# Performance work log

Hardware: AMD Instinct MI355X
Metric: run time of the kernel (lower is better)

## Reference

```python
import math
import jax, jax.numpy as jnp
import numpy as np

B, N, C, H = 64, 197, 768, 12
KEEP_RATE = 0.7

def setup_inputs() -> dict:
    key = jax.random.key(0)
    k0, k1, k2 = jax.random.split(key, 3)
    x = jax.random.normal(k0, (B, N, C), jnp.float32)
    qkv_w = jax.random.normal(k1, (C, 3 * C), jnp.float32) * 0.02
    qkv_b = jnp.zeros((3 * C,), jnp.float32)
    proj_w = jax.random.normal(k2, (C, C), jnp.float32) * 0.02
    proj_b = jnp.zeros((C,), jnp.float32)
    return {"x": x, "qkv_w": qkv_w, "qkv_b": qkv_b, "proj_w": proj_w, "proj_b": proj_b}

def reference(x, qkv_w, qkv_b, proj_w, proj_b):
    b, n, c = x.shape
    d = c // H
    scale = d ** -0.5
    # qkv: [B,N,3C] -> [3,B,H,N,d]
    qkv = (x @ qkv_w + qkv_b).reshape(b, n, 3, H, d)
    qkv = jnp.transpose(qkv, (2, 0, 3, 1, 4))
    q, k, v = qkv[0], qkv[1], qkv[2]
    attn = jax.nn.softmax(jnp.einsum('bhnd,bhmd->bhnm', q, k) * scale, axis=-1)  # [B,H,N,N]
    out = jnp.einsum('bhnm,bhmd->bhnd', attn, v)          # [B,H,N,d]
    out = jnp.transpose(out, (0, 2, 1, 3)).reshape(b, n, c)
    x_out = out @ proj_w + proj_b                          # [B,N,C]
    # dynamic token pruning via CLS attention (row 0, excluding CLS itself)
    left_tokens = math.ceil(KEEP_RATE * (n - 1))
    cls_attn = attn[:, :, 0, 1:].mean(axis=1)              # [B,N-1]
    _, idx = jax.lax.top_k(cls_attn, left_tokens)          # descending, sorted
    index = jnp.broadcast_to(idx[:, :, None], (b, left_tokens, c))
    return (x_out, index, idx, cls_attn, left_tokens)
```

## Files before the change

kernel.cpp:

```cpp
#include <hip/hip_runtime.h>
#include <math.h>

#define BB   64
#define NTOK 197
#define CC   768
#define HH   12
#define DH   64
#define MTOT (BB * NTOK)
#define MPAD 12672
#define LEFT 138

#define XOUT_OFF  0
#define INDEX_OFF 9682944
#define IDX_OFF   16465920
#define CLS_OFF   16474752
#define LT_OFF    16487296

typedef short s8v __attribute__((ext_vector_type(8)));
typedef short s4v __attribute__((ext_vector_type(4)));
typedef float f4v __attribute__((ext_vector_type(4)));

#define GLOAD16(g, l) __builtin_amdgcn_global_load_lds( \
    (const __attribute__((address_space(1))) unsigned int*)(g), \
    (__attribute__((address_space(3))) unsigned int*)(l), 16, 0, 0)

__device__ __forceinline__ unsigned short f2bf(float f) {
    union { float f; unsigned int i; } x; x.f = f;
    unsigned int r = x.i + 0x7FFFu + ((x.i >> 16) & 1u);
    return (unsigned short)(r >> 16);
}

__global__ __launch_bounds__(256)
void convert_x(const float* __restrict__ in, unsigned short* __restrict__ outb)
{
    size_t i = ((size_t)blockIdx.x * 256 + threadIdx.x) * 8;
    float4 a = *(const float4*)(in + i);
    float4 b = *(const float4*)(in + i + 4);
    s8v r;
    r[0] = (short)f2bf(a.x); r[1] = (short)f2bf(a.y);
    r[2] = (short)f2bf(a.z); r[3] = (short)f2bf(a.w);
    r[4] = (short)f2bf(b.x); r[5] = (short)f2bf(b.y);
    r[6] = (short)f2bf(b.z); r[7] = (short)f2bf(b.w);
    *(s8v*)(outb + i) = r;
}

__global__ __launch_bounds__(256)
void transpose_w2(const float* __restrict__ inq, const float* __restrict__ inp,
                  unsigned short* __restrict__ outq, unsigned short* __restrict__ outp)
{
    __shared__ float tile[32][33];
    const int bi = blockIdx.x;
    int bj = blockIdx.y;
    const float* in; unsigned short* outb; int N;
    if (bj < 72) { in = inq; outb = outq; N = 2304; }
    else         { bj -= 72; in = inp; outb = outp; N = 768; }
    const int tx = threadIdx.x & 31, ty = threadIdx.x >> 5;
#pragma unroll
    for (int r = ty; r < 32; r += 8)
        tile[r][tx] = in[(size_t)(bi * 32 + r) * N + bj * 32 + tx];
    __syncthreads();
#pragma unroll
    for (int r = ty; r < 32; r += 8)
        outb[(size_t)(bj * 32 + r) * 768 + bi * 32 + tx] = f2bf(tile[tx][r]);
}

__global__ __launch_bounds__(256, 3)
void gemm_bf16(const unsigned short* __restrict__ A, const unsigned short* __restrict__ BT,
               const float* __restrict__ bias, int ncolt, int mode, int rt0, int nrt,
               unsigned short* __restrict__ outb, float* __restrict__ outf)
{
    const int id = blockIdx.x;
    const int xcd = id & 7;
    const int t = id >> 3;
    const int ct = t % ncolt, s = t / ncolt;
    const int rt = s * 8 + xcd;
    if (rt >= nrt) return;
    const int m0 = (rt0 + rt) * 128, n0 = ct * 128;

    const int tid = threadIdx.x;
    const int wave = tid >> 6, lane = tid & 63;
    const int quad = lane >> 4, l16 = lane & 15;
    const int rowbase = (wave >> 1) * 64, colbase = (wave & 1) * 64;
    __shared__ __align__(16) short As[128 * 64];
    __shared__ __align__(16) short Bs[128 * 64];

    const int rA   = lane >> 3;
    const int gcol = ((lane & 7) ^ rA) * 8;
    unsigned int agof[4], bgof[4];
#pragma unroll
    for (int i = 0; i < 4; ++i) {
        int c = wave * 4 + i;
        agof[i] = (unsigned int)((m0 + c * 8 + rA) * 768 + gcol);
        bgof[i] = (unsigned int)((n0 + c * 8 + rA) * 768 + gcol);
    }
    int aoff[4], boff[4];
#pragma unroll
    for (int i = 0; i < 4; ++i) {
        aoff[i] = (rowbase + i * 16 + l16) * 64 + ((quad ^ (l16 & 7)) * 8);
        boff[i] = (colbase + i * 16 + l16) * 64 + ((quad ^ (l16 & 7)) * 8);
    }

    f4v acc[4][4];
#pragma unroll
    for (int i = 0; i < 4; ++i)
#pragma unroll
        for (int j = 0; j < 4; ++j) acc[i][j] = (f4v)0.f;

    for (int k0 = 0; k0 < 768; k0 += 64) {
#pragma unroll
        for (int i = 0; i < 4; ++i) {
            int c = wave * 4 + i;
            GLOAD16(A  + agof[i] + k0, &As[c * 512]);
            GLOAD16(BT + bgof[i] + k0, &Bs[c * 512]);
        }
        __syncthreads();
#pragma unroll
        for (int ks = 0; ks < 2; ++ks) {
            const int x = ks * 32;
            s8v af[4], bf[4];
#pragma unroll
            for (int i = 0; i < 4; ++i) af[i] = *(const s8v*)&As[aoff[i] ^ x];
#pragma unroll
            for (int j = 0; j < 4; ++j) bf[j] = *(const s8v*)&Bs[boff[j] ^ x];
#pragma unroll
            for (int i = 0; i < 4; ++i)
#pragma unroll
                for (int j = 0; j < 4; ++j)
                    acc[i][j] = __builtin_amdgcn_mfma_f32_16x16x32_bf16(bf[j], af[i], acc[i][j], 0, 0, 0);
        }
        __syncthreads();
    }

    const int ncols = mode ? 768 : 2304;
#pragma unroll
    for (int i = 0; i < 4; ++i) {
        const int m = m0 + rowbase + i * 16 + l16;
        if (m >= MTOT) continue;
#pragma unroll
        for (int j = 0; j < 4; ++j) {
            const int nb = n0 + colbase + j * 16 + quad * 4;
            float4 b4 = *(const float4*)&bias[nb];
            if (mode == 1) {
                float4 r;
                r.x = acc[i][j][0] + b4.x; r.y = acc[i][j][1] + b4.y;
                r.z = acc[i][j][2] + b4.z; r.w = acc[i][j][3] + b4.w;
                *(float4*)(outf + (size_t)m * ncols + nb) = r;
            } else {
                s4v r;
                r[0] = (short)f2bf(acc[i][j][0] + b4.x);
                r[1] = (short)f2bf(acc[i][j][1] + b4.y);
                r[2] = (short)f2bf(acc[i][j][2] + b4.z);
                r[3] = (short)f2bf(acc[i][j][3] + b4.w);
                *(s4v*)(outb + (size_t)m * ncols + nb) = r;
            }
        }
    }
}

#define VTS 224

__global__ __launch_bounds__(256)
void transpose_v(const unsigned short* __restrict__ qkv, unsigned short* __restrict__ vt)
{
    __shared__ short tile[32][33];
    const int bx = blockIdx.x;
    const int by = blockIdx.y;
    const int bh = blockIdx.z;
    const int b = bh / HH, h = bh - b * HH;
    const int tx = threadIdx.x & 31, ty = threadIdx.x >> 5;
    const unsigned short* vin = qkv + (size_t)b * NTOK * 2304 + 1536 + h * DH;
#pragma unroll
    for (int r = ty; r < 32; r += 8) {
        const int tok = bx * 32 + r;
        tile[r][tx] = (tok < NTOK) ? (short)vin[(size_t)tok * 2304 + by * 32 + tx] : (short)0;
    }
    __syncthreads();
#pragma unroll
    for (int r = ty; r < 32; r += 8) {
        const int d = by * 32 + r;
        vt[((size_t)bh * DH + d) * VTS + bx * 32 + tx] = tile[tx][r];
    }
}

#define PSTR 226

__global__ __launch_bounds__(256, 2)
void attn_mfma4(const unsigned short* __restrict__ qkv, const unsigned short* __restrict__ vt,
                unsigned short* __restrict__ attnbf)
{
    const int bh = blockIdx.x;
    const int g  = blockIdx.y;
    const int b = bh / HH, h = bh - b * HH;
    const int tid = threadIdx.x;
    const int wave = tid >> 6, lane = tid & 63;
    const int quad = lane >> 4, l16 = lane & 15;
    __shared__ __align__(16) short Ks[NTOK * 64];
    __shared__ short Ps[4][16 * PSTR];

    const unsigned short* qg = qkv + (size_t)b * NTOK * 2304 + h * DH;
    const unsigned short* kg = qg + 768;
    const unsigned short* vtb = vt + (size_t)bh * DH * VTS;

    for (int u = tid; u < NTOK * 8; u += 256) {
        const int row = u >> 3, seg = u & 7;
        *(s8v*)&Ks[row * 64 + (seg ^ (row & 7)) * 8] =
            *(const s8v*)(kg + (size_t)row * 2304 + seg * 8);
    }
    __syncthreads();

    const int strip = g * 4 + wave;
    if (strip >= 13) return;

    const int mq = min(strip * 16 + l16, NTOK - 1);
    const s8v aq0 = *(const s8v*)(qg + (size_t)mq * 2304 + quad * 8);
    const s8v aq1 = *(const s8v*)(qg + (size_t)mq * 2304 + 32 + quad * 8);

    f4v sacc[14];
#pragma unroll
    for (int j = 0; j < 14; ++j) sacc[j] = (f4v)0.f;
    __builtin_amdgcn_s_setprio(1);
#pragma unroll
    for (int j = 0; j < 14; ++j) {
        const int kt = min(j * 16 + l16, NTOK - 1);
        s8v bk0 = *(const s8v*)&Ks[kt * 64 + ((quad       ^ (kt & 7)) * 8)];
        s8v bk1 = *(const s8v*)&Ks[kt * 64 + (((quad + 4) ^ (kt & 7)) * 8)];
        sacc[j] = __builtin_amdgcn_mfma_f32_16x16x32_bf16(bk0, aq0, sacc[j], 0, 0, 0);
        sacc[j] = __builtin_amdgcn_mfma_f32_16x16x32_bf16(bk1, aq1, sacc[j], 0, 0, 0);
    }
    __builtin_amdgcn_s_setprio(0);

    s8v bvr[7][4];
#pragma unroll
    for (int t = 0; t < 7; ++t) {
        const int ko = t * 32 + quad * 8;
#pragma unroll
        for (int j = 0; j < 4; ++j)
            bvr[t][j] = *(const s8v*)(vtb + (size_t)(j * 16 + l16) * VTS + ko);
    }

    float mx = -1e30f;
#pragma unroll
    for (int j = 0; j < 14; ++j)
#pragma unroll
        for (int r = 0; r < 4; ++r) {
            const int key = j * 16 + quad * 4 + r;
            float s = (key < NTOK) ? sacc[j][r] * 0.125f : -1e30f;
            sacc[j][r] = s;
            mx = fmaxf(mx, s);
        }
    mx = fmaxf(mx, __shfl_xor(mx, 16, 64));
    mx = fmaxf(mx, __shfl_xor(mx, 32, 64));

    float sm = 0.f;
#pragma unroll
    for (int j = 0; j < 14; ++j) {
        s4v pk;
#pragma unroll
        for (int r = 0; r < 4; ++r) {
            const int key = j * 16 + quad * 4 + r;
            float p = (key < NTOK) ? __expf(sacc[j][r] - mx) : 0.f;
            sm += p;
            pk[r] = (short)f2bf(p);
        }
        *(s4v*)&Ps[wave][l16 * PSTR + j * 16 + quad * 4] = pk;
    }
    sm += __shfl_xor(sm, 16, 64);
    sm += __shfl_xor(sm, 32, 64);
    const float rcp = 1.f / sm;

    f4v oacc[4];
#pragma unroll
    for (int j = 0; j < 4; ++j) oacc[j] = (f4v)0.f;
    __builtin_amdgcn_s_setprio(1);
#pragma unroll
    for (int t = 0; t < 7; ++t) {
        const int ko = t * 32 + quad * 8;
        s8v ap = *(const s8v*)&Ps[wave][l16 * PSTR + ko];
#pragma unroll
        for (int j = 0; j < 4; ++j)
            oacc[j] = __builtin_amdgcn_mfma_f32_16x16x32_bf16(bvr[t][j], ap, oacc[j], 0, 0, 0);
    }
    __builtin_amdgcn_s_setprio(0);
    const int qrow = strip * 16 + l16;
    if (qrow < NTOK) {
#pragma unroll
        for (int j = 0; j < 4; ++j) {
            s4v o4;
#pragma unroll
            for (int r = 0; r < 4; ++r) o4[r] = (short)f2bf(oacc[j][r] * rcp);
            *(s4v*)&attnbf[((size_t)b * NTOK + qrow) * 768 + h * DH + j * 16 + quad * 4] = o4;
        }
    }
}

#define QCH  64
#define BGRP 8

__global__ __launch_bounds__(256)
void qr_kernel(const float* __restrict__ x, const float* __restrict__ qkv_w,
               const float* __restrict__ qkv_b, float* __restrict__ rws,
               float* __restrict__ bconst)
{
    const int h  = blockIdx.x;
    const int b0 = blockIdx.y * BGRP;
    const int tid = threadIdx.x;
    __shared__ float x0s[BGRP][CC];
    __shared__ float wbuf[2][QCH * DH];
    __shared__ float q0s[BGRP][DH];

    for (int u = tid; u < BGRP * CC; u += 256) {
        int b = u / CC, c = u - b * CC;
        x0s[b][c] = x[(size_t)(b0 + b) * NTOK * CC + c];
    }
    for (int u = tid; u < QCH * DH; u += 256) {
        int cc = u >> 6, dd = u & 63;
        wbuf[0][u] = qkv_w[(size_t)cc * 2304 + h * DH + dd];
    }
    __syncthreads();

    const int d  = tid & 63;
    const int bA = tid >> 6;
    const int bB = bA + 4;
    float accA = qkv_b[h * DH + d];
    float accB = qkv_b[h * DH + d];
    for (int k = 0; k < CC / QCH; ++k) {
        const int cur = k & 1;
        if (k + 1 < CC / QCH) {
            const int cbase = (k + 1) * QCH;
            for (int u = tid; u < QCH * DH; u += 256) {
                int cc = u >> 6, dd = u & 63;
                wbuf[cur ^ 1][u] = qkv_w[(size_t)(cbase + cc) * 2304 + h * DH + dd];
            }
        }
        const int cb = k * QCH;
#pragma unroll
        for (int cc = 0; cc < QCH; ++cc) {
            const float wv = wbuf[cur][cc * 64 + d];
            accA = fmaf(x0s[bA][cb + cc], wv, accA);
            accB = fmaf(x0s[bB][cb + cc], wv, accB);
        }
        __syncthreads();
    }
    q0s[bA][d] = accA;
    q0s[bB][d] = accB;
    __syncthreads();

    if (tid < BGRP) {
        float acc3 = 0.f;
        for (int dd = 0; dd < DH; ++dd) acc3 += q0s[tid][dd] * qkv_b[CC + h * DH + dd];
        bconst[(b0 + tid) * HH + h] = acc3;
    }

    for (int c = tid; c < CC; c += 256) {
        const float* wrow = qkv_w + (size_t)c * 2304 + CC + h * DH;
        float acc2[BGRP];
#pragma unroll
        for (int b = 0; b < BGRP; ++b) acc2[b] = 0.f;
#pragma unroll
        for (int dd = 0; dd < DH; dd += 4) {
            float4 w4 = *(const float4*)(wrow + dd);
#pragma unroll
            for (int b = 0; b < BGRP; ++b) {
                acc2[b] = fmaf(w4.x, q0s[b][dd + 0], acc2[b]);
                acc2[b] = fmaf(w4.y, q0s[b][dd + 1], acc2[b]);
                acc2[b] = fmaf(w4.z, q0s[b][dd + 2], acc2[b]);
                acc2[b] = fmaf(w4.w, q0s[b][dd + 3], acc2[b]);
            }
        }
#pragma unroll
        for (int b = 0; b < BGRP; ++b)
            rws[((size_t)(b0 + b) * HH + h) * CC + c] = acc2[b];
    }
}

#define CTOK 22
#define CCH  96
#define CSTR 100

__global__ __launch_bounds__(256)
void cls_s(const float* __restrict__ x, const float* __restrict__ rws,
           const float* __restrict__ bconst, float* __restrict__ sws)
{
    const int b = blockIdx.y;
    const int tid = threadIdx.x;
    __shared__ __align__(16) float rl[HH * 772];
    __shared__ float bcs[HH];
    __shared__ __align__(16) float xt[2][CTOK * CSTR];

    for (int u = tid; u < HH * CC; u += 256) {
        int h = u / CC, c = u - h * CC;
        rl[h * 772 + c] = rws[(size_t)b * HH * CC + u];
    }
    if (tid < HH) bcs[tid] = bconst[b * HH + tid];

    const int pair0 = blockIdx.x * 256;
    const int tok0 = pair0 / HH;
    const int local = pair0 + tid;
    const int tok = local / HH;
    const int h = local - tok * HH;
    const bool act = (local < NTOK * HH);
    const int trow = tok - tok0;

    for (int u = tid; u < CTOK * (CCH / 4); u += 256) {
        const int row = u / (CCH / 4), c4 = u - row * (CCH / 4);
        const int tk = tok0 + row;
        if (tk < NTOK)
            *(float4*)&xt[0][row * CSTR + c4 * 4] =
                *(const float4*)(x + ((size_t)b * NTOK + tk) * CC + c4 * 4);
    }
    __syncthreads();

    float acc = 0.f;
    for (int ch = 0; ch < CC / CCH; ++ch) {
        const int cur = ch & 1;
        if (ch + 1 < CC / CCH) {
            const int cb = (ch + 1) * CCH;
            for (int u = tid; u < CTOK * (CCH / 4); u += 256) {
                const int row = u / (CCH / 4), c4 = u - row * (CCH / 4);
                const int tk = tok0 + row;
                if (tk < NTOK)
                    *(float4*)&xt[cur ^ 1][row * CSTR + c4 * 4] =
                        *(const float4*)(x + ((size_t)b * NTOK + tk) * CC + cb + c4 * 4);
            }
        }
        if (act) {
            const float* xr = &xt[cur][trow * CSTR];
            const float* rp = rl + h * 772 + ch * CCH;
#pragma unroll
            for (int c = 0; c < CCH; c += 4) {
                float4 x4 = *(const float4*)(xr + c);
                float4 r4 = *(const float4*)(rp + c);
                acc = fmaf(x4.x, r4.x, acc);
                acc = fmaf(x4.y, r4.y, acc);
                acc = fmaf(x4.z, r4.z, acc);
                acc = fmaf(x4.w, r4.w, acc);
            }
        }
        __syncthreads();
    }
    if (act)
        sws[((size_t)b * HH + h) * NTOK + tok] = (acc + bcs[h]) * 0.125f;
}

__global__ __launch_bounds__(256)
void cls_topk(const float* __restrict__ sws, float* __restrict__ out, int write_lt)
{
    const int b = blockIdx.x, tid = threadIdx.x;
    const int wave = tid >> 6, lane = tid & 63;
    __shared__ float sbuf[HH][208];
    __shared__ float pm[4][208];
    __shared__ float vals[256];
    __shared__ int   idxs[256];

    for (int jj = lane; jj < 208; jj += 64) pm[wave][jj] = 0.f;
    if (tid < NTOK) {
#pragma unroll
        for (int h = 0; h < HH; ++h)
            sbuf[h][tid] = sws[((size_t)b * HH + h) * NTOK + tid];
    }
    __syncthreads();

    for (int h = wave; h < HH; h += 4) {
        float sv[4], ev[4];
        float mx = -1e30f;
#pragma unroll
        for (int t = 0; t < 4; ++t) {
            int j = lane + 64 * t;
            sv[t] = (j < NTOK) ? sbuf[h][j] : -1e30f;
            mx = fmaxf(mx, sv[t]);
        }
#pragma unroll
        for (int off = 1; off < 64; off <<= 1) mx = fmaxf(mx, __shfl_xor(mx, off, 64));
        float sm = 0.f;
#pragma unroll
        for (int t = 0; t < 4; ++t) {
            int j = lane + 64 * t;
            ev[t] = (j < NTOK) ? expf(sv[t] - mx) : 0.f;
            sm += ev[t];
        }
#pragma unroll
        for (int off = 1; off < 64; off <<= 1) sm += __shfl_xor(sm, off, 64);
#pragma unroll
        for (int t = 0; t < 4; ++t) {
            int j = lane + 64 * t;
            if (j < NTOK) pm[wave][j] += ev[t] / sm;
        }
    }
    __syncthreads();

    float v = -INFINITY;
    int id = 256 + tid;
    if (tid < NTOK - 1) {
        int j = tid + 1;
        float s = ((pm[0][j] + pm[1][j]) + (pm[2][j] + pm[3][j])) * (1.f / 12.f);
        v = s; id = tid;
        out[CLS_OFF + (size_t)b * (NTOK - 1) + tid] = s;
    }
    vals[tid] = v; idxs[tid] = id;
    __syncthreads();

    for (int k = 2; k <= 256; k <<= 1) {
        for (int j = k >> 1; j > 0; j >>= 1) {
            int ixj = tid ^ j;
            if (ixj > tid) {
                float va = vals[tid], vb2 = vals[ixj];
                int ia = idxs[tid], ib = idxs[ixj];
                bool aLess = (va > vb2) || (va == vb2 && ia < ib);
                bool dir = ((tid & k) == 0);
                if (dir != aLess) {
                    vals[tid] = vb2; vals[ixj] = va;
                    idxs[tid] = ib;  idxs[ixj] = ia;
                }
            }
            __syncthreads();
        }
    }

    if (tid < LEFT) out[IDX_OFF + (size_t)b * LEFT + tid] = (float)idxs[tid];
    if (write_lt && b == 0 && tid == 0) out[LT_OFF] = (float)LEFT;
}

__global__ __launch_bounds__(64)
void write_index(const float* __restrict__ idx_in, float* __restrict__ out)
{
    const int row = blockIdx.x;
    const float v = idx_in[row];
    const int tid = threadIdx.x;
    float4 r; r.x = v; r.y = v; r.z = v; r.w = v;
#pragma unroll
    for (int i = 0; i < 3; ++i)
        *(float4*)(out + INDEX_OFF + (size_t)row * CC + (tid + 64 * i) * 4) = r;
}

extern "C" void kernel_launch(void* const* d_in, const int* in_sizes, int n_in,
                              void* d_out, int out_size, void* d_ws, size_t ws_size,
                              hipStream_t stream)
{
    const float* x      = (const float*)d_in[0];
    const float* qkv_w  = (const float*)d_in[1];
    const float* qkv_b  = (const float*)d_in[2];
    const float* proj_w = (const float*)d_in[3];
    const float* proj_b = (const float*)d_in[4];
    float* out = (float*)d_out;

    char* w = (char*)d_ws;
    unsigned short* xbf   = (unsigned short*)w; w += (size_t)MPAD * CC * 2;
    unsigned short* wt1   = (unsigned short*)w; w += (size_t)3 * CC * CC * 2;
    unsigned short* wt2   = (unsigned short*)w; w += (size_t)CC * CC * 2;
    unsigned short* qkvbf = (unsigned short*)w; w += (size_t)MTOT * 3 * CC * 2;
    unsigned short* atbf  = (unsigned short*)w; w += (size_t)MPAD * CC * 2;
    float* rws    = (float*)w; w += (size_t)BB * HH * CC * 4;
    float* bconst = (float*)w; w += (size_t)BB * HH * 4;
    float* sws    = (float*)w; w += (size_t)BB * HH * NTOK * 4;
    unsigned short* vtbf  = (unsigned short*)d_ws;

    convert_x<<<dim3(4728), 256, 0, stream>>>(x, xbf);
    transpose_w2<<<dim3(24, 96), 256, 0, stream>>>(qkv_w, proj_w, wt1, wt2);
    qr_kernel<<<dim3(HH, BB / BGRP), 256, 0, stream>>>(x, qkv_w, qkv_b, rws, bconst);
    cls_s<<<dim3(10, 64), 256, 0, stream>>>(x, rws, bconst, sws);
    cls_topk<<<dim3(BB), 256, 0, stream>>>(sws, out, (out_size > LT_OFF) ? 1 : 0);
    write_index<<<dim3(BB * LEFT), 64, 0, stream>>>(out + IDX_OFF, out);
    gemm_bf16<<<dim3(8 * 18 * 7), 256, 0, stream>>>(xbf, wt1, qkv_b, 18, 0, 0, 50, qkvbf, nullptr);
    gemm_bf16<<<dim3(8 * 18 * 7), 256, 0, stream>>>(xbf, wt1, qkv_b, 18, 0, 50, 49, qkvbf, nullptr);
    transpose_v<<<dim3(7, 2, BB * HH), 256, 0, stream>>>(qkvbf, vtbf);
    attn_mfma4<<<dim3(BB * HH, 4), 256, 0, stream>>>(qkvbf, vtbf, atbf);
    gemm_bf16<<<dim3(8 * 6 * 13), 256, 0, stream>>>(atbf, wt2, proj_b, 6, 1, 0, 99,
                                                    nullptr, out + XOUT_OFF);
}
```

Before: 353.4 us.

## Use one 8-wave block per head for attention and merge QKV GEMM launches

The attention kernel goes from four 256-thread blocks per (batch, head), each staging all of K in LDS, to a single 512-thread block per head. Each of its 8 waves loops over query strips and reads K and V^T straight from global memory instead of from LDS or a register preload. This removes the K staging repeated across blocks, a barrier, and most of the LDS use, which should allow more resident blocks. The two split QKV GEMM launches become one launch over all row tiles, saving a launch. The cost is more global/L2 traffic for K and V fragments, and waves 0-4 do two strips while the others do one, so the block's waves are unevenly loaded.

```diff
diff --git a/kernel.cpp b/kernel.cpp
--- a/kernel.cpp
+++ b/kernel.cpp
@@ -184,111 +184,94 @@
 
 #define PSTR 226
 
-__global__ __launch_bounds__(256, 2)
-void attn_mfma4(const unsigned short* __restrict__ qkv, const unsigned short* __restrict__ vt,
-                unsigned short* __restrict__ attnbf)
+__global__ __launch_bounds__(512, 4)
+void attn8(const unsigned short* __restrict__ qkv, const unsigned short* __restrict__ vt,
+           unsigned short* __restrict__ attnbf)
 {
     const int bh = blockIdx.x;
-    const int g  = blockIdx.y;
     const int b = bh / HH, h = bh - b * HH;
     const int tid = threadIdx.x;
     const int wave = tid >> 6, lane = tid & 63;
     const int quad = lane >> 4, l16 = lane & 15;
-    __shared__ __align__(16) short Ks[NTOK * 64];
-    __shared__ short Ps[4][16 * PSTR];
+    __shared__ short Ps[8][16 * PSTR];
 
     const unsigned short* qg = qkv + (size_t)b * NTOK * 2304 + h * DH;
     const unsigned short* kg = qg + 768;
     const unsigned short* vtb = vt + (size_t)bh * DH * VTS;
 
-    for (int u = tid; u < NTOK * 8; u += 256) {
-        const int row = u >> 3, seg = u & 7;
-        *(s8v*)&Ks[row * 64 + (seg ^ (row & 7)) * 8] =
-            *(const s8v*)(kg + (size_t)row * 2304 + seg * 8);
-    }
-    __syncthreads();
-
-    const int strip = g * 4 + wave;
-    if (strip >= 13) return;
-
-    const int mq = min(strip * 16 + l16, NTOK - 1);
-    const s8v aq0 = *(const s8v*)(qg + (size_t)mq * 2304 + quad * 8);
-    const s8v aq1 = *(const s8v*)(qg + (size_t)mq * 2304 + 32 + quad * 8);
-
-    f4v sacc[14];
-#pragma unroll
-    for (int j = 0; j < 14; ++j) sacc[j] = (f4v)0.f;
-    __builtin_amdgcn_s_setprio(1);
-#pragma unroll
-    for (int j = 0; j < 14; ++j) {
-        const int kt = min(j * 16 + l16, NTOK - 1);
-        s8v bk0 = *(const s8v*)&Ks[kt * 64 + ((quad       ^ (kt & 7)) * 8)];
-        s8v bk1 = *(const s8v*)&Ks[kt * 64 + (((quad + 4) ^ (kt & 7)) * 8)];
-        sacc[j] = __builtin_amdgcn_mfma_f32_16x16x32_bf16(bk0, aq0, sacc[j], 0, 0, 0);
-        sacc[j] = __builtin_amdgcn_mfma_f32_16x16x32_bf16(bk1, aq1, sacc[j], 0, 0, 0);
-    }
-    __builtin_amdgcn_s_setprio(0);
-
-    s8v bvr[7][4];
-#pragma unroll
-    for (int t = 0; t < 7; ++t) {
-        const int ko = t * 32 + quad * 8;
-#pragma unroll
-        for (int j = 0; j < 4; ++j)
-            bvr[t][j] = *(const s8v*)(vtb + (size_t)(j * 16 + l16) * VTS + ko);
-    }
-
-    float mx = -1e30f;
-#pragma unroll
-    for (int j = 0; j < 14; ++j)
-#pragma unroll
-        for (int r = 0; r < 4; ++r) {
-            const int key = j * 16 + quad * 4 + r;
-            float s = (key < NTOK) ? sacc[j][r] * 0.125f : -1e30f;
-            sacc[j][r] = s;
-            mx = fmaxf(mx, s);
-        }
-    mx = fmaxf(mx, __shfl_xor(mx, 16, 64));
-    mx = fmaxf(mx, __shfl_xor(mx, 32, 64));
-
-    float sm = 0.f;
-#pragma unroll
-    for (int j = 0; j < 14; ++j) {
-        s4v pk;
-#pragma unroll
-        for (int r = 0; r < 4; ++r) {
-            const int key = j * 16 + quad * 4 + r;
-            float p = (key < NTOK) ? __expf(sacc[j][r] - mx) : 0.f;
-            sm += p;
-            pk[r] = (short)f2bf(p);
-        }
-        *(s4v*)&Ps[wave][l16 * PSTR + j * 16 + quad * 4] = pk;
-    }
-    sm += __shfl_xor(sm, 16, 64);
-    sm += __shfl_xor(sm, 32, 64);
-    const float rcp = 1.f / sm;
-
-    f4v oacc[4];
-#pragma unroll
-    for (int j = 0; j < 4; ++j) oacc[j] = (f4v)0.f;
-    __builtin_amdgcn_s_setprio(1);
-#pragma unroll
-    for (int t = 0; t < 7; ++t) {
-        const int ko = t * 32 + quad * 8;
-        s8v ap = *(const s8v*)&Ps[wave][l16 * PSTR + ko];
-#pragma unroll
-        for (int j = 0; j < 4; ++j)
-            oacc[j] = __builtin_amdgcn_mfma_f32_16x16x32_bf16(bvr[t][j], ap, oacc[j], 0, 0, 0);
-    }
-    __builtin_amdgcn_s_setprio(0);
-    const int qrow = strip * 16 + l16;
-    if (qrow < NTOK) {
-#pragma unroll
-        for (int j = 0; j < 4; ++j) {
-            s4v o4;
-#pragma unroll
-            for (int r = 0; r < 4; ++r) o4[r] = (short)f2bf(oacc[j][r] * rcp);
-            *(s4v*)&attnbf[((size_t)b * NTOK + qrow) * 768 + h * DH + j * 16 + quad * 4] = o4;
+    for (int strip = wave; strip < 13; strip += 8) {
+        const int mq = min(strip * 16 + l16, NTOK - 1);
+        const s8v aq0 = *(const s8v*)(qg + (size_t)mq * 2304 + quad * 8);
+        const s8v aq1 = *(const s8v*)(qg + (size_t)mq * 2304 + 32 + quad * 8);
+
+        f4v sacc[14];
+#pragma unroll
+        for (int j = 0; j < 14; ++j) sacc[j] = (f4v)0.f;
+        __builtin_amdgcn_s_setprio(1);
+#pragma unroll
+        for (int j = 0; j < 14; ++j) {
+            const int kt = min(j * 16 + l16, NTOK - 1);
+            s8v bk0 = *(const s8v*)(kg + (size_t)kt * 2304 + quad * 8);
+            s8v bk1 = *(const s8v*)(kg + (size_t)kt * 2304 + 32 + quad * 8);
+            sacc[j] = __builtin_amdgcn_mfma_f32_16x16x32_bf16(bk0, aq0, sacc[j], 0, 0, 0);
+            sacc[j] = __builtin_amdgcn_mfma_f32_16x16x32_bf16(bk1, aq1, sacc[j], 0, 0, 0);
+        }
+        __builtin_amdgcn_s_setprio(0);
+
+        float mx = -1e30f;
+#pragma unroll
+        for (int j = 0; j < 14; ++j)
+#pragma unroll
+            for (int r = 0; r < 4; ++r) {
+                const int key = j * 16 + quad * 4 + r;
+                float s = (key < NTOK) ? sacc[j][r] * 0.125f : -1e30f;
+                sacc[j][r] = s;
+                mx = fmaxf(mx, s);
+            }
+        mx = fmaxf(mx, __shfl_xor(mx, 16, 64));
+        mx = fmaxf(mx, __shfl_xor(mx, 32, 64));
+
+        float sm = 0.f;
+#pragma unroll
+        for (int j = 0; j < 14; ++j) {
+            s4v pk;
+#pragma unroll
+            for (int r = 0; r < 4; ++r) {
+                const int key = j * 16 + quad * 4 + r;
+                float p = (key < NTOK) ? __expf(sacc[j][r] - mx) : 0.f;
+                sm += p;
+                pk[r] = (short)f2bf(p);
+            }
+            *(s4v*)&Ps[wave][l16 * PSTR + j * 16 + quad * 4] = pk;
+        }
+        sm += __shfl_xor(sm, 16, 64);
+        sm += __shfl_xor(sm, 32, 64);
+        const float rcp = 1.f / sm;
+
+        f4v oacc[4];
+#pragma unroll
+        for (int j = 0; j < 4; ++j) oacc[j] = (f4v)0.f;
+        __builtin_amdgcn_s_setprio(1);
+#pragma unroll
+        for (int t = 0; t < 7; ++t) {
+            const int ko = t * 32 + quad * 8;
+            s8v ap = *(const s8v*)&Ps[wave][l16 * PSTR + ko];
+#pragma unroll
+            for (int j = 0; j < 4; ++j) {
+                s8v bv = *(const s8v*)(vtb + (size_t)(j * 16 + l16) * VTS + ko);
+                oacc[j] = __builtin_amdgcn_mfma_f32_16x16x32_bf16(bv, ap, oacc[j], 0, 0, 0);
+            }
+        }
+        __builtin_amdgcn_s_setprio(0);
+        const int qrow = strip * 16 + l16;
+        if (qrow < NTOK) {
+#pragma unroll
+            for (int j = 0; j < 4; ++j) {
+                s4v o4;
+#pragma unroll
+                for (int r = 0; r < 4; ++r) o4[r] = (short)f2bf(oacc[j][r] * rcp);
+                *(s4v*)&attnbf[((size_t)b * NTOK + qrow) * 768 + h * DH + j * 16 + quad * 4] = o4;
+            }
         }
     }
 }
@@ -560,10 +543,9 @@
     cls_s<<<dim3(10, 64), 256, 0, stream>>>(x, rws, bconst, sws);
     cls_topk<<<dim3(BB), 256, 0, stream>>>(sws, out, (out_size > LT_OFF) ? 1 : 0);
     write_index<<<dim3(BB * LEFT), 64, 0, stream>>>(out + IDX_OFF, out);
-    gemm_bf16<<<dim3(8 * 18 * 7), 256, 0, stream>>>(xbf, wt1, qkv_b, 18, 0, 0, 50, qkvbf, nullptr);
-    gemm_bf16<<<dim3(8 * 18 * 7), 256, 0, stream>>>(xbf, wt1, qkv_b, 18, 0, 50, 49, qkvbf, nullptr);
+    gemm_bf16<<<dim3(8 * 18 * 13), 256, 0, stream>>>(xbf, wt1, qkv_b, 18, 0, 0, 99, qkvbf, nullptr);
     transpose_v<<<dim3(7, 2, BB * HH), 256, 0, stream>>>(qkvbf, vtbf);
-    attn_mfma4<<<dim3(BB * HH, 4), 256, 0, stream>>>(qkvbf, vtbf, atbf);
+    attn8<<<dim3(BB * HH), 512, 0, stream>>>(qkvbf, vtbf, atbf);
     gemm_bf16<<<dim3(8 * 6 * 13), 256, 0, stream>>>(atbf, wt2, proj_b, 6, 1, 0, 99,
                                                     nullptr, out + XOUT_OFF);
 }
```

Measured after the change: 477.4 us. +35.1%, slower.
